# Optimization experiments

Measured on AMD Instinct MI355X. Metric: run time of the kernel, lower is better.

## Reference

```python
import jax, jax.numpy as jnp
import numpy as np

B, N, DEG = 256, 16384, 32  # batch, num_neurons, fan-in per neuron

def setup_inputs() -> dict:
    key = jax.random.key(0)
    kx, kw, ki = jax.random.split(key, 3)
    x = jax.random.normal(kx, (B, N), dtype=jnp.float32)
    w = jax.random.normal(kw, (N, DEG), dtype=jnp.float32)  # nonzero weights per neuron
    idx = jax.random.randint(ki, (N, DEG), 0, N)            # source-neuron indices per neuron
    return {"x": x, "w": w, "idx": idx}

def reference(x, w, idx):
    # Per neuron j: gather its fan-in channels and apply Dense(1) with
    # kernel = nonzero weights, then relu; concat over neurons == axis N.
    gathered = x[:, idx]                      # [B, N, DEG] gather
    out = jnp.einsum('bnd,nd->bn', gathered, w)  # sparse matvec per batch row
    return jax.nn.relu(out)                   # [B, N]
```

## Files before the change

kernel.cpp:

```cpp
#include <hip/hip_runtime.h>


#define B      256
#define N      16384
#define DEG    32
#define NT     32
#define NCHUNK 4
#define CB     64

typedef float v4f __attribute__((ext_vector_type(4)));
typedef _Float16 h8v __attribute__((ext_vector_type(8)));

__global__ __launch_bounds__(256) void chunk_transpose_f16_kernel(
    const float* __restrict__ x, _Float16* __restrict__ xc) {
    __shared__ float tile[64][65];
    const int t     = threadIdx.x;
    const int j0    = blockIdx.x * 64;
    const int chunk = blockIdx.y;
    const int c4 = t & 15;
    const int r  = t >> 4;

#pragma unroll
    for (int it = 0; it < 4; ++it) {
        const int row = r + it * 16;
        const float4 v = *(const float4*)&x[(size_t)(chunk * 64 + row) * N + j0 + 4 * c4];
        tile[row][4 * c4 + 0] = v.x;
        tile[row][4 * c4 + 1] = v.y;
        tile[row][4 * c4 + 2] = v.z;
        tile[row][4 * c4 + 3] = v.w;
    }
    __syncthreads();

    const int wv = t >> 6, l = t & 63;
    const int a  = l & 7;
    _Float16* dst = xc + (size_t)chunk * N * CB + 8 * a;
#pragma unroll
    for (int p = 0; p < 2; ++p) {
        const int j = p * 32 + wv * 8 + (l >> 3);
        h8v h;
#pragma unroll
        for (int k = 0; k < 8; ++k) h[k] = (_Float16)tile[8 * a + k][j];
        *(h8v*)&dst[(size_t)(j0 + j) * CB] = h;
    }
}

__global__ __launch_bounds__(256, 8) void gather_dot_f16_kernel(
    const _Float16* __restrict__ xc, const float* __restrict__ w,
    const int* __restrict__ idx, float* __restrict__ out) {
    __shared__ __align__(16) float smem[64 * 33];
    int*   sidx = (int*)smem;
    float* sw   = smem + 1024;

    const int t     = threadIdx.x;
    const int chunk = blockIdx.x & 3;
    const int nb    = (int)(blockIdx.x >> 2) * NT;
    const int wv    = t >> 6;
    const int l     = t & 63;
    const int slot  = wv * 8 + (l >> 3);
    const int a     = l & 7;

    {
        const int n_l = t >> 3, d4 = t & 7;
        ((int4*)sidx)[d4 * 32 + n_l] = ((const int4*)(idx + (size_t)nb * DEG))[t];
        ((float4*)sw)[d4 * 32 + n_l] = ((const float4*)(w + (size_t)nb * DEG))[t];
    }
    __syncthreads();

    const _Float16* xcb = xc + (size_t)chunk * N * CB + 8 * a;

    float acc[8] = {0.f, 0.f, 0.f, 0.f, 0.f, 0.f, 0.f, 0.f};
#pragma unroll
    for (int d4 = 0; d4 < DEG / 4; ++d4) {
        const int4   j4 = ((const int4*)sidx)[d4 * 32 + slot];
        const float4 w4 = ((const float4*)sw)[d4 * 32 + slot];
        const h8v v0 = *(const h8v*)&xcb[(size_t)j4.x * CB];
        const h8v v1 = *(const h8v*)&xcb[(size_t)j4.y * CB];
        const h8v v2 = *(const h8v*)&xcb[(size_t)j4.z * CB];
        const h8v v3 = *(const h8v*)&xcb[(size_t)j4.w * CB];
#pragma unroll
        for (int k = 0; k < 8; ++k) acc[k] = fmaf(w4.x, (float)v0[k], acc[k]);
#pragma unroll
        for (int k = 0; k < 8; ++k) acc[k] = fmaf(w4.y, (float)v1[k], acc[k]);
#pragma unroll
        for (int k = 0; k < 8; ++k) acc[k] = fmaf(w4.z, (float)v2[k], acc[k]);
#pragma unroll
        for (int k = 0; k < 8; ++k) acc[k] = fmaf(w4.w, (float)v3[k], acc[k]);
    }
    __syncthreads();

    float* tile = smem;
#pragma unroll
    for (int k = 0; k < 8; ++k)
        tile[(8 * a + k) * 33 + slot] = acc[k];
    __syncthreads();

#pragma unroll
    for (int p = 0; p < 2; ++p) {
        const int b = wv * 16 + p * 8 + (l >> 3);
        const int c = l & 7;
        v4f v;
        v.x = fmaxf(tile[b * 33 + 4 * c + 0], 0.f);
        v.y = fmaxf(tile[b * 33 + 4 * c + 1], 0.f);
        v.z = fmaxf(tile[b * 33 + 4 * c + 2], 0.f);
        v.w = fmaxf(tile[b * 33 + 4 * c + 3], 0.f);
        __builtin_nontemporal_store(v, (v4f*)&out[(size_t)(chunk * CB + b) * N + nb + 4 * c]);
    }
}

extern "C" void kernel_launch(void* const* d_in, const int* in_sizes, int n_in,
                              void* d_out, int out_size, void* d_ws, size_t ws_size,
                              hipStream_t stream) {
    const float* x   = (const float*)d_in[0];
    const float* w   = (const float*)d_in[1];
    const int*   idx = (const int*)d_in[2];
    float* out = (float*)d_out;
    _Float16* xc = (_Float16*)d_ws;

    dim3 tgrid(N / 64, B / 64);
    chunk_transpose_f16_kernel<<<tgrid, 256, 0, stream>>>(x, xc);

    gather_dot_f16_kernel<<<(N / NT) * NCHUNK, 256, 0, stream>>>(xc, w, idx, out);
}
```

Baseline: 90.86 us.

## Stage two batch rows of x in LDS and gather from shared memory

The x transpose kernel is replaced by a prep kernel that packs index pairs as 16-bit values and weights as fp16 pairs into a d-major layout. The main kernel loads two batch rows of x into LDS as packed fp16 pairs and does the 32-way gather from LDS instead of global memory, writing ReLU outputs directly. This removes the scattered global gathers and the transposed x copy. The cost is that every block rereads the packed index/weight stream, occupancy is limited by a 64KB LDS footprint, and precision drops because the weights are now fp16 too.

Result: slower. 96.67 us (+6.4%).

```diff
diff --git a/kernel.cpp b/kernel.cpp
--- a/kernel.cpp
+++ b/kernel.cpp
@@ -1,109 +1,100 @@
 #include <hip/hip_runtime.h>
 
 
-#define B      256
-#define N      16384
-#define DEG    32
-#define NT     32
-#define NCHUNK 4
-#define CB     64
+#define NB   16384
+#define DEG  32
 
-typedef float v4f __attribute__((ext_vector_type(4)));
-typedef _Float16 h8v __attribute__((ext_vector_type(8)));
+typedef __fp16 hp2 __attribute__((ext_vector_type(2)));
 
-__global__ __launch_bounds__(256) void chunk_transpose_f16_kernel(
-    const float* __restrict__ x, _Float16* __restrict__ xc) {
-    __shared__ float tile[64][65];
-    const int t     = threadIdx.x;
-    const int j0    = blockIdx.x * 64;
-    const int chunk = blockIdx.y;
-    const int c4 = t & 15;
-    const int r  = t >> 4;
+__global__ __launch_bounds__(256) void prep_pw_kernel(
+    const int* __restrict__ idx, const float* __restrict__ w,
+    uint2* __restrict__ pw) {
+    __shared__ int   idx_s[64][33];
+    __shared__ float w_s[64][33];
+    const int t  = threadIdx.x;
+    const int nb = blockIdx.x * 64;
 
+    const int4*   src  = (const int4*)(idx + (size_t)nb * DEG);
+    const float4* srcw = (const float4*)(w   + (size_t)nb * DEG);
 #pragma unroll
-    for (int it = 0; it < 4; ++it) {
-        const int row = r + it * 16;
-        const float4 v = *(const float4*)&x[(size_t)(chunk * 64 + row) * N + j0 + 4 * c4];
-        tile[row][4 * c4 + 0] = v.x;
-        tile[row][4 * c4 + 1] = v.y;
-        tile[row][4 * c4 + 2] = v.z;
-        tile[row][4 * c4 + 3] = v.w;
+    for (int p = 0; p < 2; ++p) {
+        const int e4 = t + 256 * p;
+        const int n0 = e4 >> 3;
+        const int c0 = (e4 & 7) * 4;
+        const int4 v = src[e4];
+        idx_s[n0][c0 + 0] = v.x; idx_s[n0][c0 + 1] = v.y;
+        idx_s[n0][c0 + 2] = v.z; idx_s[n0][c0 + 3] = v.w;
+        const float4 f = srcw[e4];
+        w_s[n0][c0 + 0] = f.x; w_s[n0][c0 + 1] = f.y;
+        w_s[n0][c0 + 2] = f.z; w_s[n0][c0 + 3] = f.w;
     }
     __syncthreads();
 
-    const int wv = t >> 6, l = t & 63;
-    const int a  = l & 7;
-    _Float16* dst = xc + (size_t)chunk * N * CB + 8 * a;
+    const int np    = t & 63;
+    const int dbase = t >> 6;
 #pragma unroll
-    for (int p = 0; p < 2; ++p) {
-        const int j = p * 32 + wv * 8 + (l >> 3);
-        h8v h;
-#pragma unroll
-        for (int k = 0; k < 8; ++k) h[k] = (_Float16)tile[8 * a + k][j];
-        *(h8v*)&dst[(size_t)(j0 + j) * CB] = h;
+    for (int k = 0; k < 4; ++k) {
+        const int d2 = dbase * 4 + k;
+        const unsigned j0 = (unsigned)idx_s[np][2 * d2];
+        const unsigned j1 = (unsigned)idx_s[np][2 * d2 + 1];
+        const hp2 wp = __builtin_amdgcn_cvt_pkrtz(w_s[np][2 * d2], w_s[np][2 * d2 + 1]);
+        uint2 o;
+        o.x = j0 | (j1 << 16);
+        o.y = __builtin_bit_cast(unsigned, wp);
+        pw[(size_t)d2 * NB + nb + np] = o;
     }
 }
 
-__global__ __launch_bounds__(256, 8) void gather_dot_f16_kernel(
-    const _Float16* __restrict__ xc, const float* __restrict__ w,
-    const int* __restrict__ idx, float* __restrict__ out) {
-    __shared__ __align__(16) float smem[64 * 33];
-    int*   sidx = (int*)smem;
-    float* sw   = smem + 1024;
+__global__ __launch_bounds__(512) void fused_gather_kernel(
+    const float* __restrict__ x, const uint2* __restrict__ pw,
+    float* __restrict__ out) {
+    __shared__ unsigned xh[NB];
+    const int t    = threadIdx.x;
+    const int bg   = (int)blockIdx.x >> 1;
+    const int half = (int)blockIdx.x & 1;
+    const int b0   = bg * 2;
+    const float* xr0 = x + (size_t)b0 * NB;
+    const float* xr1 = xr0 + NB;
 
-    const int t     = threadIdx.x;
-    const int chunk = blockIdx.x & 3;
-    const int nb    = (int)(blockIdx.x >> 2) * NT;
-    const int wv    = t >> 6;
-    const int l     = t & 63;
-    const int slot  = wv * 8 + (l >> 3);
-    const int a     = l & 7;
-
-    {
-        const int n_l = t >> 3, d4 = t & 7;
-        ((int4*)sidx)[d4 * 32 + n_l] = ((const int4*)(idx + (size_t)nb * DEG))[t];
-        ((float4*)sw)[d4 * 32 + n_l] = ((const float4*)(w + (size_t)nb * DEG))[t];
+#pragma unroll
+    for (int p = 0; p < 8; ++p) {
+        const int j = 4 * (t + 512 * p);
+        const float4 a0 = *(const float4*)&xr0[j];
+        const float4 a1 = *(const float4*)&xr1[j];
+        uint4 o;
+        o.x = __builtin_bit_cast(unsigned, (hp2)__builtin_amdgcn_cvt_pkrtz(a0.x, a1.x));
+        o.y = __builtin_bit_cast(unsigned, (hp2)__builtin_amdgcn_cvt_pkrtz(a0.y, a1.y));
+        o.z = __builtin_bit_cast(unsigned, (hp2)__builtin_amdgcn_cvt_pkrtz(a0.z, a1.z));
+        o.w = __builtin_bit_cast(unsigned, (hp2)__builtin_amdgcn_cvt_pkrtz(a0.w, a1.w));
+        *(uint4*)&xh[j] = o;
     }
     __syncthreads();
 
-    const _Float16* xcb = xc + (size_t)chunk * N * CB + 8 * a;
+    const int nbase = half * 8192;
+#pragma unroll 2
+    for (int i = 0; i < 16; ++i) {
+        const int n = nbase + t + 512 * i;
+        uint2 q[16];
+#pragma unroll
+        for (int d2 = 0; d2 < 16; ++d2)
+            q[d2] = pw[(size_t)d2 * NB + n];
 
-    float acc[8] = {0.f, 0.f, 0.f, 0.f, 0.f, 0.f, 0.f, 0.f};
+        float acc0 = 0.f, acc1 = 0.f;
 #pragma unroll
-    for (int d4 = 0; d4 < DEG / 4; ++d4) {
-        const int4   j4 = ((const int4*)sidx)[d4 * 32 + slot];
-        const float4 w4 = ((const float4*)sw)[d4 * 32 + slot];
-        const h8v v0 = *(const h8v*)&xcb[(size_t)j4.x * CB];
-        const h8v v1 = *(const h8v*)&xcb[(size_t)j4.y * CB];
-        const h8v v2 = *(const h8v*)&xcb[(size_t)j4.z * CB];
-        const h8v v3 = *(const h8v*)&xcb[(size_t)j4.w * CB];
-#pragma unroll
-        for (int k = 0; k < 8; ++k) acc[k] = fmaf(w4.x, (float)v0[k], acc[k]);
-#pragma unroll
-        for (int k = 0; k < 8; ++k) acc[k] = fmaf(w4.y, (float)v1[k], acc[k]);
-#pragma unroll
-        for (int k = 0; k < 8; ++k) acc[k] = fmaf(w4.z, (float)v2[k], acc[k]);
-#pragma unroll
-        for (int k = 0; k < 8; ++k) acc[k] = fmaf(w4.w, (float)v3[k], acc[k]);
-    }
-    __syncthreads();
-
-    float* tile = smem;
-#pragma unroll
-    for (int k = 0; k < 8; ++k)
-        tile[(8 * a + k) * 33 + slot] = acc[k];
-    __syncthreads();
-
-#pragma unroll
-    for (int p = 0; p < 2; ++p) {
-        const int b = wv * 16 + p * 8 + (l >> 3);
-        const int c = l & 7;
-        v4f v;
-        v.x = fmaxf(tile[b * 33 + 4 * c + 0], 0.f);
-        v.y = fmaxf(tile[b * 33 + 4 * c + 1], 0.f);
-        v.z = fmaxf(tile[b * 33 + 4 * c + 2], 0.f);
-        v.w = fmaxf(tile[b * 33 + 4 * c + 3], 0.f);
-        __builtin_nontemporal_store(v, (v4f*)&out[(size_t)(chunk * CB + b) * N + nb + 4 * c]);
+        for (int d2 = 0; d2 < 16; ++d2) {
+            const unsigned jp = q[d2].x;
+            const unsigned r0 = xh[jp & 0xffffu];
+            const unsigned r1 = xh[jp >> 16];
+            const hp2 w2 = __builtin_bit_cast(hp2, q[d2].y);
+            const hp2 p0 = __builtin_bit_cast(hp2, r0);
+            const hp2 p1 = __builtin_bit_cast(hp2, r1);
+            acc0 = fmaf((float)w2.x, (float)p0.x, acc0);
+            acc1 = fmaf((float)w2.x, (float)p0.y, acc1);
+            acc0 = fmaf((float)w2.y, (float)p1.x, acc0);
+            acc1 = fmaf((float)w2.y, (float)p1.y, acc1);
+        }
+        out[(size_t)b0 * NB + n]       = fmaxf(acc0, 0.f);
+        out[(size_t)(b0 + 1) * NB + n] = fmaxf(acc1, 0.f);
     }
 }
 
@@ -114,10 +105,9 @@
     const float* w   = (const float*)d_in[1];
     const int*   idx = (const int*)d_in[2];
     float* out = (float*)d_out;
-    _Float16* xc = (_Float16*)d_ws;
+    uint2* pw  = (uint2*)d_ws;
 
-    dim3 tgrid(N / 64, B / 64);
-    chunk_transpose_f16_kernel<<<tgrid, 256, 0, stream>>>(x, xc);
+    prep_pw_kernel<<<NB / 64, 256, 0, stream>>>(idx, w, pw);
 
-    gather_dot_f16_kernel<<<(N / NT) * NCHUNK, 256, 0, stream>>>(xc, w, idx, out);
+    fused_gather_kernel<<<256, 512, 0, stream>>>(x, pw, out);
 }
```
